# Kernel tuning notes

Measured on AMD Instinct MI355X. Metric: run time of the kernel, lower is better.

The kernel has to match this reference:

```python
import jax, jax.numpy as jnp
import numpy as np

N_NODES = 50000
N_EDGES = 800000
IN_DIM = 256
HID = 64
NEG_SLOPE = 0.2


def setup_inputs() -> dict:
    key = jax.random.key(0)
    ks = jax.random.split(key, 16)
    s = lambda d: 1.0 / np.sqrt(d)
    x = jax.random.normal(ks[0], (N_NODES, IN_DIM), dtype=jnp.float32)
    src = jax.random.randint(ks[1], (N_EDGES,), 0, N_NODES, dtype=jnp.int32)
    dst = jax.random.randint(ks[2], (N_EDGES,), 0, N_NODES, dtype=jnp.int32)
    # layer 0: in 256 -> 4 heads x 64, no residual, ELU
    W0 = jax.random.normal(ks[3], (IN_DIM, 4 * HID), dtype=jnp.float32) * s(IN_DIM)
    al0 = jax.random.normal(ks[4], (4, HID), dtype=jnp.float32) * s(HID)
    ar0 = jax.random.normal(ks[5], (4, HID), dtype=jnp.float32) * s(HID)
    b0 = jnp.zeros((4 * HID,), dtype=jnp.float32)
    # layer 1: in 256 -> 4 heads x 64, identity residual (256 == 4*64), ELU
    W1 = jax.random.normal(ks[6], (4 * HID, 4 * HID), dtype=jnp.float32) * s(4 * HID)
    al1 = jax.random.normal(ks[7], (4, HID), dtype=jnp.float32) * s(HID)
    ar1 = jax.random.normal(ks[8], (4, HID), dtype=jnp.float32) * s(HID)
    b1 = jnp.zeros((4 * HID,), dtype=jnp.float32)
    # layer 2 (output): in 256 -> 1 head x 64, linear residual, no activation
    W2 = jax.random.normal(ks[9], (4 * HID, HID), dtype=jnp.float32) * s(4 * HID)
    al2 = jax.random.normal(ks[10], (1, HID), dtype=jnp.float32) * s(HID)
    ar2 = jax.random.normal(ks[11], (1, HID), dtype=jnp.float32) * s(HID)
    b2 = jnp.zeros((HID,), dtype=jnp.float32)
    res_w2 = jax.random.normal(ks[12], (4 * HID, HID), dtype=jnp.float32) * s(4 * HID)
    return {"x": x, "src": src, "dst": dst,
            "W0": W0, "al0": al0, "ar0": ar0, "b0": b0,
            "W1": W1, "al1": al1, "ar1": ar1, "b1": b1,
            "W2": W2, "al2": al2, "ar2": ar2, "b2": b2,
            "res_w2": res_w2}


def gat_layer(h, src, dst, W, al, ar, bias, residual, res_w, activation):
    H, D = al.shape
    feat = (h @ W).reshape(-1, H, D)               # [N,H,D]
    el = jnp.sum(feat * al[None], axis=-1)         # [N,H]
    er = jnp.sum(feat * ar[None], axis=-1)         # [N,H]
    e = jax.nn.leaky_relu(el[src] + er[dst], NEG_SLOPE)  # [E,H]
    # segment softmax over incoming edges of each destination node
    emax = jax.ops.segment_max(e, dst, num_segments=N_NODES)  # [N,H]
    ee = jnp.exp(e - emax[dst])
    denom = jax.ops.segment_sum(ee, dst, num_segments=N_NODES)
    alpha = ee / denom[dst]                        # [E,H]
    msg = feat[src] * alpha[..., None]             # [E,H,D]
    out = jax.ops.segment_sum(msg, dst, num_segments=N_NODES)  # [N,H,D]
    if residual:
        if res_w is not None:
            out = out + (h @ res_w).reshape(-1, 1, D)
        else:
            out = out + h.reshape(-1, H, D)
    out = out + bias.reshape(H, D)
    if activation:
        out = jax.nn.elu(out)
    return out.reshape(-1, H * D)                  # flatten(1)


def reference(x, src, dst, W0, al0, ar0, b0, W1, al1, ar1, b1,
              W2, al2, ar2, b2, res_w2):
    h = gat_layer(x, src, dst, W0, al0, ar0, b0, False, None, True)
    h = gat_layer(h, src, dst, W1, al1, ar1, b1, True, None, True)
    h = gat_layer(h, src, dst, W2, al2, ar2, b2, True, res_w2, False)
    return h  # [N, 64]
```

## Files before the change

kernel.cpp:

```cpp
#include <hip/hip_runtime.h>
#include <math.h>

#define NNODES 50000
#define NEDGES 800000
#define NSB 49

__device__ __forceinline__ float leaky(float x) { return x > 0.f ? x : 0.2f * x; }

__device__ __forceinline__ ushort f2bf(float f) {
    unsigned u = __float_as_uint(f);
    return (ushort)((u + 0x7fffu + ((u >> 16) & 1u)) >> 16);
}
__device__ __forceinline__ float bf2f(ushort u) {
    return __uint_as_float((unsigned)u << 16);
}

typedef const __attribute__((address_space(1))) void* gptr_t;
typedef __attribute__((address_space(3))) void* lptr_t;

__global__ void hist_kernel(const int* __restrict__ dst, int* __restrict__ counts) {
    int e = blockIdx.x * 256 + threadIdx.x;
    if (e < NEDGES) atomicAdd(&counts[dst[e]], 1);
}

__global__ __launch_bounds__(256) void prep_kernel(
    const int* __restrict__ counts, int* __restrict__ bsum, int Nn,
    const float* __restrict__ W0, const float* __restrict__ W1, const float* __restrict__ W2,
    const float* __restrict__ Wr, ushort* __restrict__ Bt0, ushort* __restrict__ Bt1,
    ushort* __restrict__ Bt2) {
    int t = threadIdx.x;
    if (blockIdx.x < NSB) {
        int b = blockIdx.x;
        int base = b * 1024;
        int v = 0;
#pragma unroll
        for (int i = 0; i < 4; ++i) {
            int idx = base + t + 256 * i;
            if (idx < Nn) v += counts[idx];
        }
        for (int o = 32; o; o >>= 1) v += __shfl_xor(v, o);
        __shared__ int ws[4];
        if ((t & 63) == 0) ws[t >> 6] = v;
        __syncthreads();
        if (t == 0) bsum[b] = ws[0] + ws[1] + ws[2] + ws[3];
    } else {
        int idx = (blockIdx.x - NSB) * 256 + t;
        if (idx < 65536) {
            int n = idx >> 8, k = idx & 255;
            Bt0[idx] = f2bf(W0[k * 256 + n]);
        } else if (idx < 131072) {
            int j = idx - 65536;
            int n = j >> 8, k = j & 255;
            Bt1[j] = f2bf(W1[k * 256 + n]);
        } else {
            int j = idx - 131072;
            int n = j >> 8, k = j & 255;
            Bt2[j] = f2bf(n < 64 ? W2[k * 64 + n] : Wr[k * 64 + (n - 64)]);
        }
    }
}

__global__ __launch_bounds__(256) void scan_final(const int* __restrict__ counts,
                                                  const int* __restrict__ bsum,
                                                  int* __restrict__ row_start, int Nn, int nB) {
    __shared__ int off_s;
    __shared__ int tsum[256];
    int b = blockIdx.x, t = threadIdx.x;
    if (t == 0) {
        int o = 0;
        for (int i = 0; i < b; ++i) o += bsum[i];
        off_s = o;
    }
    int base = b * 1024 + t * 4;
    int c0 = 0, c1 = 0, c2 = 0, c3 = 0;
    if (base + 3 < Nn) {
        int4 c = *reinterpret_cast<const int4*>(counts + base);
        c0 = c.x; c1 = c.y; c2 = c.z; c3 = c.w;
    } else {
        if (base + 0 < Nn) c0 = counts[base + 0];
        if (base + 1 < Nn) c1 = counts[base + 1];
        if (base + 2 < Nn) c2 = counts[base + 2];
        if (base + 3 < Nn) c3 = counts[base + 3];
    }
    int s0 = c0, s1 = s0 + c1, s2 = s1 + c2, s3 = s2 + c3;
    tsum[t] = s3;
    __syncthreads();
    for (int o = 1; o < 256; o <<= 1) {
        int u = (t >= o) ? tsum[t - o] : 0;
        __syncthreads();
        tsum[t] += u;
        __syncthreads();
    }
    int o = off_s + tsum[t] - s3;
    if (base + 3 < Nn) {
        *reinterpret_cast<int4*>(row_start + base) = make_int4(o, o + s0, o + s1, o + s2);
    } else {
        if (base + 0 < Nn) row_start[base + 0] = o;
        if (base + 1 < Nn) row_start[base + 1] = o + s0;
        if (base + 2 < Nn) row_start[base + 2] = o + s1;
        if (base + 3 < Nn) row_start[base + 3] = o + s2;
    }
    if (b == nB - 1 && t == 255) row_start[Nn] = off_s + tsum[255];
}

__global__ void scatter_kernel(const int* __restrict__ src, const int* __restrict__ dst,
                               const int* __restrict__ row_start, int* __restrict__ cursor,
                               int* __restrict__ csr_src) {
    int e = blockIdx.x * 256 + threadIdx.x;
    if (e < NEDGES) {
        int d = dst[e];
        int pos = row_start[d] + atomicAdd(&cursor[d], 1);
        csr_src[pos] = src[e];
    }
}

template <int MCOLS, bool ABF16>
__global__ __launch_bounds__(256) void gemm_mfma(const void* __restrict__ Araw,
                                                 const ushort* __restrict__ Bt,
                                                 const float* __restrict__ al,
                                                 const float* __restrict__ ar,
                                                 ushort* __restrict__ featb,
                                                 float* __restrict__ el, float* __restrict__ er,
                                                 float* __restrict__ resid, int Nrows) {
    using bf16x8 = __attribute__((ext_vector_type(8))) short;
    using f32x4 = __attribute__((ext_vector_type(4))) float;
    __shared__ ushort As[8192];
    __shared__ ushort Bs[8192];
    const float* Af = (const float*)Araw;
    const ushort* Ab = (const ushort*)Araw;
    const int tid = threadIdx.x;
    const int lane = tid & 63;
    const int wave = tid >> 6;
    const int wr = wave >> 1, wc = wave & 1;
    const int q = lane >> 4, li = lane & 15;
    const int r0 = blockIdx.x * 128;
    const int n0 = blockIdx.y * 128;

    f32x4 acc[4][4];
#pragma unroll
    for (int i = 0; i < 4; ++i)
#pragma unroll
        for (int j = 0; j < 4; ++j) acc[i][j] = (f32x4){0.f, 0.f, 0.f, 0.f};

    for (int kk = 0; kk < 256; kk += 64) {
        __syncthreads();
        if constexpr (ABF16) {
#pragma unroll
            for (int j = 0; j < 4; ++j) {
                int c = (wave * 4 + j) * 64 + lane;
                int mr = c & 15, kg = (c >> 4) & 7, mf = c >> 7;
                const ushort* gp = Ab + (size_t)(r0 + mf * 16 + mr) * 256 + kk + kg * 8;
                void* lp = (char*)As + (size_t)(wave * 4 + j) * 1024;
                __builtin_amdgcn_global_load_lds((gptr_t)gp, (lptr_t)lp, 16, 0, 0);
            }
        } else {
#pragma unroll
            for (int j = 0; j < 4; ++j) {
                int g = j * 256 + tid;
                int m = g >> 3, kg = g & 7;
                int mf = m >> 4, mr = m & 15;
                int row = r0 + m;
                float4 v0 = make_float4(0.f, 0.f, 0.f, 0.f), v1 = v0;
                if (row < Nrows) {
                    const float* p = Af + (size_t)row * 256 + kk + kg * 8;
                    v0 = *reinterpret_cast<const float4*>(p);
                    v1 = *reinterpret_cast<const float4*>(p + 4);
                }
                union { bf16x8 v; ushort u[8]; } pk;
                pk.u[0] = f2bf(v0.x); pk.u[1] = f2bf(v0.y);
                pk.u[2] = f2bf(v0.z); pk.u[3] = f2bf(v0.w);
                pk.u[4] = f2bf(v1.x); pk.u[5] = f2bf(v1.y);
                pk.u[6] = f2bf(v1.z); pk.u[7] = f2bf(v1.w);
                *reinterpret_cast<bf16x8*>(&As[((mf * 8 + kg) * 16 + (mr ^ kg)) * 8]) = pk.v;
            }
        }
#pragma unroll
        for (int j = 0; j < 4; ++j) {
            int c = (wave * 4 + j) * 64 + lane;
            int nr = c & 15, kg = (c >> 4) & 7, nf = c >> 7;
            const ushort* gp = Bt + (size_t)(n0 + nf * 16 + nr) * 256 + kk + kg * 8;
            void* lp = (char*)Bs + (size_t)(wave * 4 + j) * 1024;
            __builtin_amdgcn_global_load_lds((gptr_t)gp, (lptr_t)lp, 16, 0, 0);
        }
        __syncthreads();
#pragma unroll
        for (int t = 0; t < 2; ++t) {
            const int kc = t * 4 + q;
            bf16x8 af[4], bfv[4];
#pragma unroll
            for (int f = 0; f < 4; ++f) {
                int ai = ABF16 ? li : (li ^ kc);
                af[f] = *reinterpret_cast<const bf16x8*>(
                    &As[(((wr * 4 + f) * 8 + kc) * 16 + ai) * 8]);
                bfv[f] = *reinterpret_cast<const bf16x8*>(
                    &Bs[(((wc * 4 + f) * 8 + kc) * 16 + li) * 8]);
            }
#pragma unroll
            for (int f = 0; f < 4; ++f)
#pragma unroll
                for (int f2 = 0; f2 < 4; ++f2)
                    acc[f][f2] =
                        __builtin_amdgcn_mfma_f32_16x16x32_bf16(af[f], bfv[f2], acc[f][f2], 0, 0, 0);
        }
    }

    if constexpr (MCOLS == 256) {
        const int hblk = (n0 >> 6) + wc;
        float alv[4], arv[4];
#pragma unroll
        for (int f2 = 0; f2 < 4; ++f2) {
            alv[f2] = al[hblk * 64 + f2 * 16 + li];
            arv[f2] = ar[hblk * 64 + f2 * 16 + li];
        }
#pragma unroll
        for (int f = 0; f < 4; ++f) {
#pragma unroll
            for (int r = 0; r < 4; ++r) {
                int row = r0 + wr * 64 + f * 16 + q * 4 + r;
                bool ok = row < Nrows;
                float elp = 0.f, erp = 0.f;
#pragma unroll
                for (int f2 = 0; f2 < 4; ++f2) {
                    float v = acc[f][f2][r];
                    elp = fmaf(v, alv[f2], elp);
                    erp = fmaf(v, arv[f2], erp);
                    if (ok) featb[(size_t)row * 256 + (f2 * 16 + li) * 4 + hblk] = f2bf(v);
                }
#pragma unroll
                for (int o = 1; o < 16; o <<= 1) {
                    elp += __shfl_xor(elp, o);
                    erp += __shfl_xor(erp, o);
                }
                if (ok && li == 0) {
                    el[row * 4 + hblk] = elp;
                    er[row * 4 + hblk] = erp;
                }
            }
        }
    } else {
        if (wc == 0) {
            float alv[4], arv[4];
#pragma unroll
            for (int f2 = 0; f2 < 4; ++f2) {
                alv[f2] = al[f2 * 16 + li];
                arv[f2] = ar[f2 * 16 + li];
            }
#pragma unroll
            for (int f = 0; f < 4; ++f) {
#pragma unroll
                for (int r = 0; r < 4; ++r) {
                    int row = r0 + wr * 64 + f * 16 + q * 4 + r;
                    bool ok = row < Nrows;
                    float elp = 0.f, erp = 0.f;
#pragma unroll
                    for (int f2 = 0; f2 < 4; ++f2) {
                        float v = acc[f][f2][r];
                        elp = fmaf(v, alv[f2], elp);
                        erp = fmaf(v, arv[f2], erp);
                        if (ok) featb[(size_t)row * 64 + f2 * 16 + li] = f2bf(v);
                    }
#pragma unroll
                    for (int o = 1; o < 16; o <<= 1) {
                        elp += __shfl_xor(elp, o);
                        erp += __shfl_xor(erp, o);
                    }
                    if (ok && li == 0) {
                        el[row] = elp;
                        er[row] = erp;
                    }
                }
            }
        } else {
#pragma unroll
            for (int f = 0; f < 4; ++f) {
#pragma unroll
                for (int r = 0; r < 4; ++r) {
                    int row = r0 + wr * 64 + f * 16 + q * 4 + r;
                    if (row < Nrows) {
#pragma unroll
                        for (int f2 = 0; f2 < 4; ++f2)
                            resid[(size_t)row * 64 + f2 * 16 + li] = acc[f][f2][r];
                    }
                }
            }
        }
    }
}

template <int RES, bool ACT>
__global__ __launch_bounds__(256) void agg4_kernel(
    const ushort* __restrict__ featb, const float* __restrict__ el,
    const float* __restrict__ er, const int* __restrict__ row_start,
    const int* __restrict__ csr_src, const ushort* __restrict__ resbuf,
    const float* __restrict__ bias, ushort* __restrict__ out, int Nn) {
    using ushort8v = __attribute__((ext_vector_type(8))) unsigned short;
    __shared__ float wbuf[4][256];
    __shared__ int obuf[4][64];
    const int wv = threadIdx.x >> 6, lane = threadIdx.x & 63;
    const int g = lane >> 5, li = lane & 31;
    int node = blockIdx.x * 4 + wv;
    if (node >= Nn) return;

    int begin = row_start[node], end = row_start[node + 1];
    float4 ern = *(reinterpret_cast<const float4*>(er) + node);

    float denom[4] = {0.f, 0.f, 0.f, 0.f};
    float acc[2][4] = {{0.f, 0.f, 0.f, 0.f}, {0.f, 0.f, 0.f, 0.f}};

    for (int c = begin; c < end; c += 64) {
        int nE = min(64, end - c);
        float4 w = make_float4(0.f, 0.f, 0.f, 0.f);
        int s = 0;
        if (lane < nE) {
            s = csr_src[c + lane];
            float4 e4 = *(reinterpret_cast<const float4*>(el) + s);
            w.x = __expf(leaky(e4.x + ern.x));
            w.y = __expf(leaky(e4.y + ern.y));
            w.z = __expf(leaky(e4.z + ern.z));
            w.w = __expf(leaky(e4.w + ern.w));
        }
        denom[0] += w.x; denom[1] += w.y; denom[2] += w.z; denom[3] += w.w;
        obuf[wv][lane] = s * 256;
        *reinterpret_cast<float4*>(&wbuf[wv][lane * 4]) = w;
        __asm__ volatile("s_waitcnt lgkmcnt(0)" ::: "memory");

#pragma unroll 4
        for (int e2 = 0; e2 < nE; e2 += 2) {
            int e = e2 + g;
            float4 we = make_float4(0.f, 0.f, 0.f, 0.f);
            int off = 0;
            if (e < nE) {
                off = obuf[wv][e];
                we = *reinterpret_cast<const float4*>(&wbuf[wv][e * 4]);
            }
            ushort8v v = *reinterpret_cast<const ushort8v*>(featb + off + li * 8);
            acc[0][0] = fmaf(we.x, bf2f(v[0]), acc[0][0]);
            acc[0][1] = fmaf(we.y, bf2f(v[1]), acc[0][1]);
            acc[0][2] = fmaf(we.z, bf2f(v[2]), acc[0][2]);
            acc[0][3] = fmaf(we.w, bf2f(v[3]), acc[0][3]);
            acc[1][0] = fmaf(we.x, bf2f(v[4]), acc[1][0]);
            acc[1][1] = fmaf(we.y, bf2f(v[5]), acc[1][1]);
            acc[1][2] = fmaf(we.z, bf2f(v[6]), acc[1][2]);
            acc[1][3] = fmaf(we.w, bf2f(v[7]), acc[1][3]);
        }
        __asm__ volatile("" ::: "memory");
    }

#pragma unroll
    for (int j = 0; j < 2; ++j)
#pragma unroll
        for (int h = 0; h < 4; ++h) acc[j][h] += __shfl_xor(acc[j][h], 32);
#pragma unroll
    for (int h = 0; h < 4; ++h)
        for (int o = 32; o; o >>= 1) denom[h] += __shfl_xor(denom[h], o);

    bool has = end > begin;
#pragma unroll
    for (int hh = 0; hh < 2; ++hh) {
        int h = g * 2 + hh;
        float d0 = denom[h];
        float o0 = has ? acc[0][h] / d0 : 0.f;
        float o1 = has ? acc[1][h] / d0 : 0.f;
        int dbase = h * 64 + li * 2;
        if constexpr (RES == 1) {
            unsigned rv = *reinterpret_cast<const unsigned*>(resbuf + (size_t)node * 256 + dbase);
            o0 += bf2f((ushort)(rv & 0xffffu));
            o1 += bf2f((ushort)(rv >> 16));
        }
        float2 bv = *reinterpret_cast<const float2*>(bias + dbase);
        o0 += bv.x; o1 += bv.y;
        if constexpr (ACT) {
            o0 = o0 > 0.f ? o0 : __expf(o0) - 1.f;
            o1 = o1 > 0.f ? o1 : __expf(o1) - 1.f;
        }
        unsigned pk = (unsigned)f2bf(o0) | ((unsigned)f2bf(o1) << 16);
        *reinterpret_cast<unsigned*>(out + (size_t)node * 256 + dbase) = pk;
    }
}

__global__ __launch_bounds__(256) void agg1_kernel(
    const ushort* __restrict__ featb, const float* __restrict__ el,
    const float* __restrict__ er, const int* __restrict__ row_start,
    const int* __restrict__ csr_src, const float* __restrict__ resbuf,
    const float* __restrict__ bias, float* __restrict__ out, int Nn) {
    __shared__ float wbuf[4][64];
    __shared__ int obuf[4][64];
    const int wv = threadIdx.x >> 6, lane = threadIdx.x & 63;
    const int g = lane >> 4, li = lane & 15;
    int node = blockIdx.x * 4 + wv;
    if (node >= Nn) return;

    int begin = row_start[node], end = row_start[node + 1];
    float ern = er[node];
    float denom = 0.f;
    float acc[4] = {0.f, 0.f, 0.f, 0.f};

    for (int c = begin; c < end; c += 64) {
        int nE = min(64, end - c);
        float w = 0.f;
        int s = 0;
        if (lane < nE) {
            s = csr_src[c + lane];
            w = __expf(leaky(el[s] + ern));
        }
        denom += w;
        obuf[wv][lane] = s * 64;
        wbuf[wv][lane] = w;
        __asm__ volatile("s_waitcnt lgkmcnt(0)" ::: "memory");

#pragma unroll 2
        for (int e4i = 0; e4i < nE; e4i += 4) {
            int e = e4i + g;
            float we = 0.f;
            int off = 0;
            if (e < nE) {
                off = obuf[wv][e];
                we = wbuf[wv][e];
            }
            ushort4 v = *reinterpret_cast<const ushort4*>(featb + off + li * 4);
            acc[0] = fmaf(we, bf2f(v.x), acc[0]);
            acc[1] = fmaf(we, bf2f(v.y), acc[1]);
            acc[2] = fmaf(we, bf2f(v.z), acc[2]);
            acc[3] = fmaf(we, bf2f(v.w), acc[3]);
        }
        __asm__ volatile("" ::: "memory");
    }

#pragma unroll
    for (int j = 0; j < 4; ++j) {
        acc[j] += __shfl_xor(acc[j], 16);
        acc[j] += __shfl_xor(acc[j], 32);
    }
    for (int o = 32; o; o >>= 1) denom += __shfl_xor(denom, o);

    if (g == 0) {
        bool has = end > begin;
        float4 rv = *reinterpret_cast<const float4*>(resbuf + (size_t)node * 64 + li * 4);
        float4 bv = *reinterpret_cast<const float4*>(bias + li * 4);
        float4 o4;
        o4.x = (has ? acc[0] / denom : 0.f) + rv.x + bv.x;
        o4.y = (has ? acc[1] / denom : 0.f) + rv.y + bv.y;
        o4.z = (has ? acc[2] / denom : 0.f) + rv.z + bv.z;
        o4.w = (has ? acc[3] / denom : 0.f) + rv.w + bv.w;
        *reinterpret_cast<float4*>(out + (size_t)node * 64 + li * 4) = o4;
    }
}

extern "C" void kernel_launch(void* const* d_in, const int* in_sizes, int n_in, void* d_out,
                              int out_size, void* d_ws, size_t ws_size, hipStream_t stream) {
    const float* x   = (const float*)d_in[0];
    const int* src   = (const int*)d_in[1];
    const int* dst   = (const int*)d_in[2];
    const float* W0  = (const float*)d_in[3];
    const float* al0 = (const float*)d_in[4];
    const float* ar0 = (const float*)d_in[5];
    const float* b0  = (const float*)d_in[6];
    const float* W1  = (const float*)d_in[7];
    const float* al1 = (const float*)d_in[8];
    const float* ar1 = (const float*)d_in[9];
    const float* b1  = (const float*)d_in[10];
    const float* W2  = (const float*)d_in[11];
    const float* al2 = (const float*)d_in[12];
    const float* ar2 = (const float*)d_in[13];
    const float* b2  = (const float*)d_in[14];
    const float* Wr2 = (const float*)d_in[15];
    float* out = (float*)d_out;

    char* w = (char*)d_ws;
    size_t off = 0;
    auto alloc = [&](size_t bytes) -> char* {
        char* p = w + off;
        off += (bytes + 255) & ~(size_t)255;
        return p;
    };
    ushort* hbuf    = (ushort*)alloc((size_t)NNODES * 256 * 2);
    ushort* featb   = (ushort*)alloc((size_t)NNODES * 256 * 2);
    float* resid    = (float*)alloc((size_t)NNODES * 64 * 4);
    float* el       = (float*)alloc((size_t)NNODES * 4 * 4);
    float* er       = (float*)alloc((size_t)NNODES * 4 * 4);
    ushort* Bt0     = (ushort*)alloc(65536 * 2);
    ushort* Bt1     = (ushort*)alloc(65536 * 2);
    ushort* Bt2     = (ushort*)alloc(32768 * 2);
    int* counts     = (int*)alloc((size_t)NNODES * 4 * 2);
    int* cursor     = counts + NNODES;
    int* row_start  = (int*)alloc((size_t)(NNODES + 1) * 4);
    int* bsum       = (int*)alloc(64 * 4);
    int* csr_src    = (int*)alloc((size_t)NEDGES * 4);

    hipMemsetAsync(counts, 0, (size_t)NNODES * 4 * 2, stream);

    const int EB = (NEDGES + 255) / 256;
    const int NB4 = (NNODES + 3) / 4;
    const int NBM = (NNODES + 127) / 128;

    hist_kernel<<<EB, 256, 0, stream>>>(dst, counts);
    prep_kernel<<<NSB + 640, 256, 0, stream>>>(counts, bsum, NNODES, W0, W1, W2, Wr2,
                                               Bt0, Bt1, Bt2);
    scan_final<<<NSB, 256, 0, stream>>>(counts, bsum, row_start, NNODES, NSB);
    scatter_kernel<<<EB, 256, 0, stream>>>(src, dst, row_start, cursor, csr_src);

    gemm_mfma<256, false><<<dim3(NBM, 2), 256, 0, stream>>>(x, Bt0, al0, ar0, featb, el, er,
                                                            nullptr, NNODES);
    agg4_kernel<0, true><<<NB4, 256, 0, stream>>>(featb, el, er, row_start, csr_src,
                                                  nullptr, b0, hbuf, NNODES);
    gemm_mfma<256, true><<<dim3(NBM, 2), 256, 0, stream>>>(hbuf, Bt1, al1, ar1, featb, el, er,
                                                           nullptr, NNODES);
    agg4_kernel<1, true><<<NB4, 256, 0, stream>>>(featb, el, er, row_start, csr_src,
                                                  hbuf, b1, hbuf, NNODES);
    gemm_mfma<128, true><<<dim3(NBM, 1), 256, 0, stream>>>(hbuf, Bt2, al2, ar2, featb, el, er,
                                                           resid, NNODES);
    agg1_kernel<<<NB4, 256, 0, stream>>>(featb, el, er, row_start, csr_src,
                                         resid, b2, out, NNODES);
}
```

Baseline: 446.9 us.

## Pre-convert x to bf16 in prep kernel and use full-width 512-thread GEMM tiles

Adds a pass in the prep kernel that converts the fp32 input x to bf16 once, so the layer-0 GEMM can stream A tiles through direct global-to-LDS loads. Replaces the two-block-per-row-tile GEMM with a 512-thread kernel covering all 256 output columns per 128-row tile. A is then read once per tile instead of twice. This costs an extra write and read of a bf16 copy of x and more LDS per block. The layer-2 GEMM is split into its own specialized kernel.

```diff
diff --git a/kernel.cpp b/kernel.cpp
--- a/kernel.cpp
+++ b/kernel.cpp
@@ -4,6 +4,8 @@
 #define NNODES 50000
 #define NEDGES 800000
 #define NSB 49
+#define NPACK 640
+#define NCVT 3125
 
 __device__ __forceinline__ float leaky(float x) { return x > 0.f ? x : 0.2f * x; }
 
@@ -27,7 +29,8 @@
     const int* __restrict__ counts, int* __restrict__ bsum, int Nn,
     const float* __restrict__ W0, const float* __restrict__ W1, const float* __restrict__ W2,
     const float* __restrict__ Wr, ushort* __restrict__ Bt0, ushort* __restrict__ Bt1,
-    ushort* __restrict__ Bt2) {
+    ushort* __restrict__ Bt2, const float* __restrict__ x, ushort* __restrict__ xb) {
+    using ushort8v = __attribute__((ext_vector_type(8))) unsigned short;
     int t = threadIdx.x;
     if (blockIdx.x < NSB) {
         int b = blockIdx.x;
@@ -43,7 +46,7 @@
         if ((t & 63) == 0) ws[t >> 6] = v;
         __syncthreads();
         if (t == 0) bsum[b] = ws[0] + ws[1] + ws[2] + ws[3];
-    } else {
+    } else if (blockIdx.x < NSB + NPACK) {
         int idx = (blockIdx.x - NSB) * 256 + t;
         if (idx < 65536) {
             int n = idx >> 8, k = idx & 255;
@@ -57,6 +60,19 @@
             int n = j >> 8, k = j & 255;
             Bt2[j] = f2bf(n < 64 ? W2[k * 64 + n] : Wr[k * 64 + (n - 64)]);
         }
+    } else {
+        size_t j = (size_t)(blockIdx.x - NSB - NPACK) * 4096 + t * 16;
+        float4 a0 = *reinterpret_cast<const float4*>(x + j);
+        float4 a1 = *reinterpret_cast<const float4*>(x + j + 4);
+        float4 a2 = *reinterpret_cast<const float4*>(x + j + 8);
+        float4 a3 = *reinterpret_cast<const float4*>(x + j + 12);
+        union { ushort8v v; ushort u[8]; } p0, p1;
+        p0.u[0] = f2bf(a0.x); p0.u[1] = f2bf(a0.y); p0.u[2] = f2bf(a0.z); p0.u[3] = f2bf(a0.w);
+        p0.u[4] = f2bf(a1.x); p0.u[5] = f2bf(a1.y); p0.u[6] = f2bf(a1.z); p0.u[7] = f2bf(a1.w);
+        p1.u[0] = f2bf(a2.x); p1.u[1] = f2bf(a2.y); p1.u[2] = f2bf(a2.z); p1.u[3] = f2bf(a2.w);
+        p1.u[4] = f2bf(a3.x); p1.u[5] = f2bf(a3.y); p1.u[6] = f2bf(a3.z); p1.u[7] = f2bf(a3.w);
+        *reinterpret_cast<ushort8v*>(xb + j) = p0.v;
+        *reinterpret_cast<ushort8v*>(xb + j + 8) = p1.v;
     }
 }
 
@@ -114,27 +130,119 @@
     }
 }
 
-template <int MCOLS, bool ABF16>
-__global__ __launch_bounds__(256) void gemm_mfma(const void* __restrict__ Araw,
+__global__ __launch_bounds__(512) void gemm_wide(const ushort* __restrict__ Ab,
                                                  const ushort* __restrict__ Bt,
                                                  const float* __restrict__ al,
                                                  const float* __restrict__ ar,
                                                  ushort* __restrict__ featb,
                                                  float* __restrict__ el, float* __restrict__ er,
-                                                 float* __restrict__ resid, int Nrows) {
+                                                 int Nrows) {
+    using bf16x8 = __attribute__((ext_vector_type(8))) short;
+    using f32x4 = __attribute__((ext_vector_type(4))) float;
+    __shared__ ushort As[8192];
+    __shared__ ushort Bs[16384];
+    const int tid = threadIdx.x;
+    const int lane = tid & 63;
+    const int wave = tid >> 6;
+    const int wr = wave >> 2, wc = wave & 3;
+    const int q = lane >> 4, li = lane & 15;
+    const int r0 = blockIdx.x * 128;
+
+    f32x4 acc[4][4];
+#pragma unroll
+    for (int i = 0; i < 4; ++i)
+#pragma unroll
+        for (int j = 0; j < 4; ++j) acc[i][j] = (f32x4){0.f, 0.f, 0.f, 0.f};
+
+    for (int kk = 0; kk < 256; kk += 64) {
+        __syncthreads();
+#pragma unroll
+        for (int j = 0; j < 2; ++j) {
+            int c = wave * 128 + j * 64 + lane;
+            int mr = c & 15, kg = (c >> 4) & 7, mf = c >> 7;
+            const ushort* gp = Ab + (size_t)(r0 + mf * 16 + mr) * 256 + kk + kg * 8;
+            void* lp = (char*)As + (size_t)(wave * 2 + j) * 1024;
+            __builtin_amdgcn_global_load_lds((gptr_t)gp, (lptr_t)lp, 16, 0, 0);
+        }
+#pragma unroll
+        for (int j = 0; j < 4; ++j) {
+            int c = wave * 256 + j * 64 + lane;
+            int nr = c & 15, kg = (c >> 4) & 7, nf = c >> 7;
+            const ushort* gp = Bt + (size_t)(nf * 16 + nr) * 256 + kk + kg * 8;
+            void* lp = (char*)Bs + (size_t)(wave * 4 + j) * 1024;
+            __builtin_amdgcn_global_load_lds((gptr_t)gp, (lptr_t)lp, 16, 0, 0);
+        }
+        __syncthreads();
+#pragma unroll
+        for (int t = 0; t < 2; ++t) {
+            const int kc = t * 4 + q;
+            bf16x8 af[4], bfv[4];
+#pragma unroll
+            for (int f = 0; f < 4; ++f) {
+                af[f] = *reinterpret_cast<const bf16x8*>(
+                    &As[(((wr * 4 + f) * 8 + kc) * 16 + li) * 8]);
+                bfv[f] = *reinterpret_cast<const bf16x8*>(
+                    &Bs[(((wc * 4 + f) * 8 + kc) * 16 + li) * 8]);
+            }
+#pragma unroll
+            for (int f = 0; f < 4; ++f)
+#pragma unroll
+                for (int f2 = 0; f2 < 4; ++f2)
+                    acc[f][f2] =
+                        __builtin_amdgcn_mfma_f32_16x16x32_bf16(af[f], bfv[f2], acc[f][f2], 0, 0, 0);
+        }
+    }
+
+    float alv[4], arv[4];
+#pragma unroll
+    for (int f2 = 0; f2 < 4; ++f2) {
+        alv[f2] = al[wc * 64 + f2 * 16 + li];
+        arv[f2] = ar[wc * 64 + f2 * 16 + li];
+    }
+#pragma unroll
+    for (int f = 0; f < 4; ++f) {
+#pragma unroll
+        for (int r = 0; r < 4; ++r) {
+            int row = r0 + wr * 64 + f * 16 + q * 4 + r;
+            bool ok = row < Nrows;
+            float elp = 0.f, erp = 0.f;
+#pragma unroll
+            for (int f2 = 0; f2 < 4; ++f2) {
+                float v = acc[f][f2][r];
+                elp = fmaf(v, alv[f2], elp);
+                erp = fmaf(v, arv[f2], erp);
+                if (ok) featb[(size_t)row * 256 + (f2 * 16 + li) * 4 + wc] = f2bf(v);
+            }
+#pragma unroll
+            for (int o = 1; o < 16; o <<= 1) {
+                elp += __shfl_xor(elp, o);
+                erp += __shfl_xor(erp, o);
+            }
+            if (ok && li == 0) {
+                el[row * 4 + wc] = elp;
+                er[row * 4 + wc] = erp;
+            }
+        }
+    }
+}
+
+__global__ __launch_bounds__(256) void gemm_l2(const ushort* __restrict__ Ab,
+                                               const ushort* __restrict__ Bt,
+                                               const float* __restrict__ al,
+                                               const float* __restrict__ ar,
+                                               ushort* __restrict__ featb,
+                                               float* __restrict__ el, float* __restrict__ er,
+                                               float* __restrict__ resid, int Nrows) {
     using bf16x8 = __attribute__((ext_vector_type(8))) short;
     using f32x4 = __attribute__((ext_vector_type(4))) float;
     __shared__ ushort As[8192];
     __shared__ ushort Bs[8192];
-    const float* Af = (const float*)Araw;
-    const ushort* Ab = (const ushort*)Araw;
     const int tid = threadIdx.x;
     const int lane = tid & 63;
     const int wave = tid >> 6;
     const int wr = wave >> 1, wc = wave & 1;
     const int q = lane >> 4, li = lane & 15;
     const int r0 = blockIdx.x * 128;
-    const int n0 = blockIdx.y * 128;
 
     f32x4 acc[4][4];
 #pragma unroll
@@ -144,41 +252,19 @@
 
     for (int kk = 0; kk < 256; kk += 64) {
         __syncthreads();
-        if constexpr (ABF16) {
-#pragma unroll
-            for (int j = 0; j < 4; ++j) {
-                int c = (wave * 4 + j) * 64 + lane;
-                int mr = c & 15, kg = (c >> 4) & 7, mf = c >> 7;
-                const ushort* gp = Ab + (size_t)(r0 + mf * 16 + mr) * 256 + kk + kg * 8;
-                void* lp = (char*)As + (size_t)(wave * 4 + j) * 1024;
-                __builtin_amdgcn_global_load_lds((gptr_t)gp, (lptr_t)lp, 16, 0, 0);
-            }
-        } else {
-#pragma unroll
-            for (int j = 0; j < 4; ++j) {
-                int g = j * 256 + tid;
-                int m = g >> 3, kg = g & 7;
-                int mf = m >> 4, mr = m & 15;
-                int row = r0 + m;
-                float4 v0 = make_float4(0.f, 0.f, 0.f, 0.f), v1 = v0;
-                if (row < Nrows) {
-                    const float* p = Af + (size_t)row * 256 + kk + kg * 8;
-                    v0 = *reinterpret_cast<const float4*>(p);
-                    v1 = *reinterpret_cast<const float4*>(p + 4);
-                }
-                union { bf16x8 v; ushort u[8]; } pk;
-                pk.u[0] = f2bf(v0.x); pk.u[1] = f2bf(v0.y);
-                pk.u[2] = f2bf(v0.z); pk.u[3] = f2bf(v0.w);
-                pk.u[4] = f2bf(v1.x); pk.u[5] = f2bf(v1.y);
-                pk.u[6] = f2bf(v1.z); pk.u[7] = f2bf(v1.w);
-                *reinterpret_cast<bf16x8*>(&As[((mf * 8 + kg) * 16 + (mr ^ kg)) * 8]) = pk.v;
-            }
+#pragma unroll
+        for (int j = 0; j < 4; ++j) {
+            int c = (wave * 4 + j) * 64 + lane;
+            int mr = c & 15, kg = (c >> 4) & 7, mf = c >> 7;
+            const ushort* gp = Ab + (size_t)(r0 + mf * 16 + mr) * 256 + kk + kg * 8;
+            void* lp = (char*)As + (size_t)(wave * 4 + j) * 1024;
+            __builtin_amdgcn_global_load_lds((gptr_t)gp, (lptr_t)lp, 16, 0, 0);
         }
 #pragma unroll
         for (int j = 0; j < 4; ++j) {
             int c = (wave * 4 + j) * 64 + lane;
             int nr = c & 15, kg = (c >> 4) & 7, nf = c >> 7;
-            const ushort* gp = Bt + (size_t)(n0 + nf * 16 + nr) * 256 + kk + kg * 8;
+            const ushort* gp = Bt + (size_t)(nf * 16 + nr) * 256 + kk + kg * 8;
             void* lp = (char*)Bs + (size_t)(wave * 4 + j) * 1024;
             __builtin_amdgcn_global_load_lds((gptr_t)gp, (lptr_t)lp, 16, 0, 0);
         }
@@ -189,9 +275,8 @@
             bf16x8 af[4], bfv[4];
 #pragma unroll
             for (int f = 0; f < 4; ++f) {
-                int ai = ABF16 ? li : (li ^ kc);
                 af[f] = *reinterpret_cast<const bf16x8*>(
-                    &As[(((wr * 4 + f) * 8 + kc) * 16 + ai) * 8]);
+                    &As[(((wr * 4 + f) * 8 + kc) * 16 + li) * 8]);
                 bfv[f] = *reinterpret_cast<const bf16x8*>(
                     &Bs[(((wc * 4 + f) * 8 + kc) * 16 + li) * 8]);
             }
@@ -204,13 +289,12 @@
         }
     }
 
-    if constexpr (MCOLS == 256) {
-        const int hblk = (n0 >> 6) + wc;
+    if (wc == 0) {
         float alv[4], arv[4];
 #pragma unroll
         for (int f2 = 0; f2 < 4; ++f2) {
-            alv[f2] = al[hblk * 64 + f2 * 16 + li];
-            arv[f2] = ar[hblk * 64 + f2 * 16 + li];
+            alv[f2] = al[f2 * 16 + li];
+            arv[f2] = ar[f2 * 16 + li];
         }
 #pragma unroll
         for (int f = 0; f < 4; ++f) {
@@ -224,7 +308,7 @@
                     float v = acc[f][f2][r];
                     elp = fmaf(v, alv[f2], elp);
                     erp = fmaf(v, arv[f2], erp);
-                    if (ok) featb[(size_t)row * 256 + (f2 * 16 + li) * 4 + hblk] = f2bf(v);
+                    if (ok) featb[(size_t)row * 64 + f2 * 16 + li] = f2bf(v);
                 }
 #pragma unroll
                 for (int o = 1; o < 16; o <<= 1) {
@@ -232,55 +316,21 @@
                     erp += __shfl_xor(erp, o);
                 }
                 if (ok && li == 0) {
-                    el[row * 4 + hblk] = elp;
-                    er[row * 4 + hblk] = erp;
+                    el[row] = elp;
+                    er[row] = erp;
                 }
             }
         }
     } else {
-        if (wc == 0) {
-            float alv[4], arv[4];
-#pragma unroll
-            for (int f2 = 0; f2 < 4; ++f2) {
-                alv[f2] = al[f2 * 16 + li];
-                arv[f2] = ar[f2 * 16 + li];
-            }
-#pragma unroll
-            for (int f = 0; f < 4; ++f) {
-#pragma unroll
-                for (int r = 0; r < 4; ++r) {
-                    int row = r0 + wr * 64 + f * 16 + q * 4 + r;
-                    bool ok = row < Nrows;
-                    float elp = 0.f, erp = 0.f;
-#pragma unroll
-                    for (int f2 = 0; f2 < 4; ++f2) {
-                        float v = acc[f][f2][r];
-                        elp = fmaf(v, alv[f2], elp);
-                        erp = fmaf(v, arv[f2], erp);
-                        if (ok) featb[(size_t)row * 64 + f2 * 16 + li] = f2bf(v);
-                    }
-#pragma unroll
-                    for (int o = 1; o < 16; o <<= 1) {
-                        elp += __shfl_xor(elp, o);
-                        erp += __shfl_xor(erp, o);
-                    }
-                    if (ok && li == 0) {
-                        el[row] = elp;
-                        er[row] = erp;
-                    }
-                }
-            }
-        } else {
-#pragma unroll
-            for (int f = 0; f < 4; ++f) {
-#pragma unroll
-                for (int r = 0; r < 4; ++r) {
-                    int row = r0 + wr * 64 + f * 16 + q * 4 + r;
-                    if (row < Nrows) {
-#pragma unroll
-                        for (int f2 = 0; f2 < 4; ++f2)
-                            resid[(size_t)row * 64 + f2 * 16 + li] = acc[f][f2][r];
-                    }
+#pragma unroll
+        for (int f = 0; f < 4; ++f) {
+#pragma unroll
+            for (int r = 0; r < 4; ++r) {
+                int row = r0 + wr * 64 + f * 16 + q * 4 + r;
+                if (row < Nrows) {
+#pragma unroll
+                    for (int f2 = 0; f2 < 4; ++f2)
+                        resid[(size_t)row * 64 + f2 * 16 + li] = acc[f][f2][r];
                 }
             }
         }
@@ -473,6 +523,7 @@
         off += (bytes + 255) & ~(size_t)255;
         return p;
     };
+    ushort* xb      = (ushort*)alloc((size_t)NNODES * 256 * 2);
     ushort* hbuf    = (ushort*)alloc((size_t)NNODES * 256 * 2);
     ushort* featb   = (ushort*)alloc((size_t)NNODES * 256 * 2);
     float* resid    = (float*)alloc((size_t)NNODES * 64 * 4);
@@ -494,21 +545,18 @@
     const int NBM = (NNODES + 127) / 128;
 
     hist_kernel<<<EB, 256, 0, stream>>>(dst, counts);
-    prep_kernel<<<NSB + 640, 256, 0, stream>>>(counts, bsum, NNODES, W0, W1, W2, Wr2,
-                                               Bt0, Bt1, Bt2);
+    prep_kernel<<<NSB + NPACK + NCVT, 256, 0, stream>>>(counts, bsum, NNODES, W0, W1, W2, Wr2,
+                                                        Bt0, Bt1, Bt2, x, xb);
     scan_final<<<NSB, 256, 0, stream>>>(counts, bsum, row_start, NNODES, NSB);
     scatter_kernel<<<EB, 256, 0, stream>>>(src, dst, row_start, cursor, csr_src);
 
-    gemm_mfma<256, false><<<dim3(NBM, 2), 256, 0, stream>>>(x, Bt0, al0, ar0, featb, el, er,
-                                                            nullptr, NNODES);
+    gemm_wide<<<NBM, 512, 0, stream>>>(xb, Bt0, al0, ar0, featb, el, er, NNODES);
     agg4_kernel<0, true><<<NB4, 256, 0, stream>>>(featb, el, er, row_start, csr_src,
                                                   nullptr, b0, hbuf, NNODES);
-    gemm_mfma<256, true><<<dim3(NBM, 2), 256, 0, stream>>>(hbuf, Bt1, al1, ar1, featb, el, er,
-                                                           nullptr, NNODES);
+    gemm_wide<<<NBM, 512, 0, stream>>>(hbuf, Bt1, al1, ar1, featb, el, er, NNODES);
     agg4_kernel<1, true><<<NB4, 256, 0, stream>>>(featb, el, er, row_start, csr_src,
                                                   hbuf, b1, hbuf, NNODES);
-    gemm_mfma<128, true><<<dim3(NBM, 1), 256, 0, stream>>>(hbuf, Bt2, al2, ar2, featb, el, er,
-                                                           resid, NNODES);
+    gemm_l2<<<NBM, 256, 0, stream>>>(hbuf, Bt2, al2, ar2, featb, el, er, resid, NNODES);
     agg1_kernel<<<NB4, 256, 0, stream>>>(featb, el, er, row_start, csr_src,
                                          resid, b2, out, NNODES);
 }
```

Result: no change. 438.8 us (-1.8%).
